# Kernel tuning notes

Hardware: AMD Instinct MI355X
Metric: run time of the kernel (lower is better)

The kernel has to match this reference:

```python
import jax, jax.numpy as jnp
import numpy as np

D_MODEL = 1024
N_HEADS = 16
D_FF = 4096
LN_EPS = 1e-5


def _layer_norm(x, g, b):
    m = jnp.mean(x, axis=-1, keepdims=True)
    v = jnp.mean((x - m) ** 2, axis=-1, keepdims=True)
    return (x - m) / jnp.sqrt(v + LN_EPS) * g + b


def setup_inputs() -> dict:
    key = jax.random.key(0)
    ks = jax.random.split(key, 16)
    s = 0.02
    d, dff = D_MODEL, D_FF
    return {
        "x": jax.random.normal(ks[0], (8, 1000, d), dtype=jnp.float32),
        # weights stored as (d_in, d_out); applied via x @ W
        "wq": jax.random.normal(ks[1], (d, d), dtype=jnp.float32) * s,
        "wk": jax.random.normal(ks[2], (d, d), dtype=jnp.float32) * s,
        "wv": jax.random.normal(ks[3], (d, d), dtype=jnp.float32) * s,
        "wo": jax.random.normal(ks[4], (d, d), dtype=jnp.float32) * s,
        "bo": jnp.zeros((d,), dtype=jnp.float32),
        "w1": jax.random.normal(ks[5], (d, dff), dtype=jnp.float32) * s,
        "b1": jnp.zeros((dff,), dtype=jnp.float32),
        "w2": jax.random.normal(ks[6], (dff, d), dtype=jnp.float32) * s,
        "b2": jnp.zeros((d,), dtype=jnp.float32),
        "g1": jnp.ones((d,), dtype=jnp.float32),
        "beta1": jnp.zeros((d,), dtype=jnp.float32),
        "g2": jnp.ones((d,), dtype=jnp.float32),
        "beta2": jnp.zeros((d,), dtype=jnp.float32),
    }


def reference(x, wq, wk, wv, wo, bo, w1, b1, w2, b2, g1, beta1, g2, beta2):
    B, S, D = x.shape
    H = N_HEADS
    dk = D // H

    # --- pre-norm attention ---
    h = _layer_norm(x, g1, beta1)
    q = (h @ wq).reshape(B, S, H, dk)
    k = (h @ wk).reshape(B, S, H, dk)
    v = (h @ wv).reshape(B, S, H, dk)
    scores = jnp.einsum('bqhd,bkhd->bhqk', q, k) / jnp.sqrt(jnp.float32(dk))
    mask = jnp.tril(jnp.ones((S, S), dtype=bool))  # causal
    scores = jnp.where(mask, scores, -jnp.inf)
    attn = jax.nn.softmax(scores, axis=-1)
    attended = jnp.einsum('bhqk,bkhd->bqhd', attn, v).reshape(B, S, D)
    x = x + attended @ wo + bo

    # --- pre-norm FFN (exact GELU, matching torch F.gelu default) ---
    h2 = _layer_norm(x, g2, beta2)
    ff = jax.nn.gelu(h2 @ w1 + b1, approximate=False) @ w2 + b2
    return x + ff
```

## Files before the change

### kernel.cpp

```cpp
#include <hip/hip_runtime.h>
#include <hip/hip_bf16.h>
#include <math.h>

#define D_MODEL 1024
#define D_FF    4096
#define N_HEADS 16
#define SEQ     1000
#define BATCH   8
#define M_TOK   (BATCH * SEQ)

typedef __bf16 bf16x8_t __attribute__((ext_vector_type(8)));
typedef short  short8_t __attribute__((ext_vector_type(8)));
typedef float  f32x4_t  __attribute__((ext_vector_type(4)));

__device__ __forceinline__ f32x4_t mfma_bf16(short8_t a, short8_t b, f32x4_t c) {
    return __builtin_amdgcn_mfma_f32_16x16x32_bf16(
        __builtin_bit_cast(bf16x8_t, a), __builtin_bit_cast(bf16x8_t, b), c, 0, 0, 0);
}

__device__ __forceinline__ unsigned short f2bf(float f) {
    union { float f; unsigned u; } x; x.f = f;
    unsigned r = (x.u + 0x7fffu + ((x.u >> 16) & 1u)) >> 16;
    return (unsigned short)r;
}

__device__ __forceinline__ float gelu_fast(float v) {
    float z = 1.5957691216f * v * fmaf(0.044715f, v * v, 1.0f);
    float e = __expf(-z);
    return v * __builtin_amdgcn_rcpf(1.0f + e);
}

__device__ __forceinline__ void gload_lds16(const void* g, void* l) {
    __builtin_amdgcn_global_load_lds(
        (const __attribute__((address_space(1))) unsigned int*)g,
        (__attribute__((address_space(3))) unsigned int*)l, 16, 0, 0);
}

__global__ __launch_bounds__(256) void prep_kernel(
    const float* __restrict__ wq, const float* __restrict__ wk,
    const float* __restrict__ wv, const float* __restrict__ wo,
    const float* __restrict__ w1, const float* __restrict__ w2,
    unsigned short* __restrict__ wqt, unsigned short* __restrict__ wkt,
    unsigned short* __restrict__ wvt, unsigned short* __restrict__ wot,
    unsigned short* __restrict__ w1t, unsigned short* __restrict__ w2t,
    const float* __restrict__ x, const float* __restrict__ g1,
    const float* __restrict__ beta1, unsigned short* __restrict__ h1) {
    int id = blockIdx.x;
    __shared__ float tile[32][33];
    __shared__ float red[8];
    if (id >= 12288) {
        int row = id - 12288, tid = threadIdx.x;
        const float4 v = ((const float4*)(x + (size_t)row * D_MODEL))[tid];
        float s  = v.x + v.y + v.z + v.w;
        float s2 = v.x * v.x + v.y * v.y + v.z * v.z + v.w * v.w;
#pragma unroll
        for (int o = 32; o > 0; o >>= 1) { s += __shfl_xor(s, o, 64); s2 += __shfl_xor(s2, o, 64); }
        int wave = tid >> 6, lane = tid & 63;
        if (lane == 0) { red[wave] = s; red[wave + 4] = s2; }
        __syncthreads();
        s  = red[0] + red[1] + red[2] + red[3];
        s2 = red[4] + red[5] + red[6] + red[7];
        float mean = s * (1.0f / D_MODEL);
        float var  = s2 * (1.0f / D_MODEL) - mean * mean;
        float rstd = rsqrtf(var + 1e-5f);
        float4 gg = ((const float4*)g1)[tid];
        float4 bb = ((const float4*)beta1)[tid];
        ushort4 o4;
        o4.x = f2bf((v.x - mean) * rstd * gg.x + bb.x);
        o4.y = f2bf((v.y - mean) * rstd * gg.y + bb.y);
        o4.z = f2bf((v.z - mean) * rstd * gg.z + bb.z);
        o4.w = f2bf((v.w - mean) * rstd * gg.w + bb.w);
        ((ushort4*)(h1 + (size_t)row * D_MODEL))[tid] = o4;
        return;
    }
    const float* w; unsigned short* wt; int Kd, Nd, bx, by;
    if (id < 4096) {
        int z = id >> 10, t = id & 1023;
        w  = z == 0 ? wq  : z == 1 ? wk  : z == 2 ? wv  : wo;
        wt = z == 0 ? wqt : z == 1 ? wkt : z == 2 ? wvt : wot;
        Kd = 1024; Nd = 1024; bx = t & 31; by = t >> 5;
    } else if (id < 8192) {
        int t = id - 4096;
        w = w1; wt = w1t; Kd = 1024; Nd = 4096; bx = t & 127; by = t >> 7;
    } else {
        int t = id - 8192;
        w = w2; wt = w2t; Kd = 4096; Nd = 1024; bx = t & 31; by = t >> 5;
    }
    int n0 = bx * 32, k0 = by * 32;
    int tx = threadIdx.x & 31, ty = threadIdx.x >> 5;
#pragma unroll
    for (int i = 0; i < 4; ++i)
        tile[ty + i * 8][tx] = w[(size_t)(k0 + ty + i * 8) * Nd + n0 + tx];
    __syncthreads();
#pragma unroll
    for (int i = 0; i < 4; ++i)
        wt[(size_t)(n0 + ty + i * 8) * Kd + k0 + tx] = f2bf(tile[tx][ty + i * 8]);
}

__global__ __launch_bounds__(256) void vtrans_kernel(const unsigned short* __restrict__ v,
                                                     unsigned short* __restrict__ vt) {
    __shared__ unsigned short tile[32][33];
    int b = blockIdx.z;
    int c0 = blockIdx.x * 32, s0 = blockIdx.y * 32;
    int tx = threadIdx.x, ty = threadIdx.y;
#pragma unroll
    for (int i = 0; i < 4; ++i) {
        int s = s0 + ty + i * 8;
        unsigned short val = 0;
        if (s < SEQ) val = v[((size_t)b * SEQ + s) * D_MODEL + c0 + tx];
        tile[ty + i * 8][tx] = val;
    }
    __syncthreads();
#pragma unroll
    for (int i = 0; i < 4; ++i) {
        int c = c0 + ty + i * 8;
        vt[((size_t)b * D_MODEL + c) * 1024 + s0 + tx] = tile[tx][ty + i * 8];
    }
}

__global__ __launch_bounds__(256) void ln_kernel(const float* __restrict__ x,
                                                 const float* __restrict__ g,
                                                 const float* __restrict__ beta,
                                                 unsigned short* __restrict__ out) {
    int row = blockIdx.x, tid = threadIdx.x;
    const float4 v = ((const float4*)(x + (size_t)row * D_MODEL))[tid];
    float s  = v.x + v.y + v.z + v.w;
    float s2 = v.x * v.x + v.y * v.y + v.z * v.z + v.w * v.w;
#pragma unroll
    for (int o = 32; o > 0; o >>= 1) { s += __shfl_xor(s, o, 64); s2 += __shfl_xor(s2, o, 64); }
    __shared__ float red[8];
    int wave = tid >> 6, lane = tid & 63;
    if (lane == 0) { red[wave] = s; red[wave + 4] = s2; }
    __syncthreads();
    s  = red[0] + red[1] + red[2] + red[3];
    s2 = red[4] + red[5] + red[6] + red[7];
    float mean = s * (1.0f / D_MODEL);
    float var  = s2 * (1.0f / D_MODEL) - mean * mean;
    float rstd = rsqrtf(var + 1e-5f);
    float4 gg = ((const float4*)g)[tid];
    float4 bb = ((const float4*)beta)[tid];
    ushort4 o4;
    o4.x = f2bf((v.x - mean) * rstd * gg.x + bb.x);
    o4.y = f2bf((v.y - mean) * rstd * gg.y + bb.y);
    o4.z = f2bf((v.z - mean) * rstd * gg.z + bb.z);
    o4.w = f2bf((v.w - mean) * rstd * gg.w + bb.w);
    ((ushort4*)(out + (size_t)row * D_MODEL))[tid] = o4;
}

enum { EPI_BF16 = 0, EPI_GELU = 1, EPI_RES_F32 = 2 };

template <int EPI, int KDIM, bool FUSE3>
__global__ __launch_bounds__(256) void gemm_bt(
    const unsigned short* __restrict__ A,
    const unsigned short* __restrict__ Bt0,
    const unsigned short* __restrict__ Bt1,
    const unsigned short* __restrict__ Bt2,
    const float* __restrict__ bias,
    const float* __restrict__ resid,
    void* __restrict__ out0, void* out1, void* out2,
    int Mdim, int Ndim) {
    constexpr int K = KDIM;
    constexpr int NKT = K / 64;
    __shared__ unsigned short lda[2][128 * 64];
    __shared__ unsigned short ldb[2][128 * 64];
    int tid = threadIdx.x;
    int lane = tid & 63, wave = tid >> 6;
    int l15 = lane & 15, quad = lane >> 4;
    int rt = blockIdx.y * 128;
    const unsigned short* Bt = Bt0;
    void* outp = out0;
    int ct;
    if (FUSE3) {
        int sel = blockIdx.x >> 3;
        ct = (blockIdx.x & 7) * 128;
        Bt   = sel == 0 ? Bt0  : (sel == 1 ? Bt1  : Bt2);
        outp = sel == 0 ? out0 : (sel == 1 ? out1 : out2);
    } else {
        ct = blockIdx.x * 128;
    }
    int wr = (wave >> 1) * 64, wc = (wave & 1) * 64;
    f32x4_t acc[4][4] = {};

    const unsigned short* ag[4];
    const unsigned short* bg[4];
#pragma unroll
    for (int i = 0; i < 4; ++i) {
        int gidx = tid + i * 256;
        int row = gidx >> 3, cp = gidx & 7;
        int c = cp ^ (row & 7);
        int ar = rt + row; if (ar >= Mdim) ar = Mdim - 1;
        ag[i] = A  + (size_t)ar * K + c * 8;
        bg[i] = Bt + (size_t)(ct + row) * K + c * 8;
    }

    auto stage = [&](int kt, int bufi) {
#pragma unroll
        for (int i = 0; i < 4; ++i) {
            gload_lds16(ag[i] + kt * 64, (char*)lda[bufi] + (wave * 64 + i * 256) * 16);
            gload_lds16(bg[i] + kt * 64, (char*)ldb[bufi] + (wave * 64 + i * 256) * 16);
        }
    };

    stage(0, 0);
    for (int kt = 0; kt < NKT; ++kt) {
        int bufi = kt & 1;
        __syncthreads();
        if (kt + 1 < NKT) stage(kt + 1, bufi ^ 1);
        const unsigned short* la = lda[bufi];
        const unsigned short* lb = ldb[bufi];
#pragma unroll
        for (int kc = 0; kc < 2; ++kc) {
            short8_t af[4], bfr[4];
#pragma unroll
            for (int mi = 0; mi < 4; ++mi) {
                int ra = wr + mi * 16 + l15;
                int cg = (kc * 4 + quad) ^ (ra & 7);
                af[mi] = *(const short8_t*)(la + (ra * 8 + cg) * 8);
            }
#pragma unroll
            for (int ni = 0; ni < 4; ++ni) {
                int rb = wc + ni * 16 + l15;
                int cg = (kc * 4 + quad) ^ (rb & 7);
                bfr[ni] = *(const short8_t*)(lb + (rb * 8 + cg) * 8);
            }
#pragma unroll
            for (int mi = 0; mi < 4; ++mi)
#pragma unroll
                for (int ni = 0; ni < 4; ++ni)
                    acc[mi][ni] = mfma_bf16(af[mi], bfr[ni], acc[mi][ni]);
        }
    }

    float bias_c[4];
    if (EPI != EPI_BF16) {
#pragma unroll
        for (int ni = 0; ni < 4; ++ni) bias_c[ni] = bias[ct + wc + ni * 16 + l15];
    }

#pragma unroll
    for (int mi = 0; mi < 4; ++mi) {
#pragma unroll
        for (int r = 0; r < 4; ++r) {
            int grow = rt + wr + mi * 16 + quad * 4 + r;
            if (grow >= Mdim) continue;
#pragma unroll
            for (int ni = 0; ni < 4; ++ni) {
                int gcol = ct + wc + ni * 16 + l15;
                float v = acc[mi][ni][r];
                size_t idx = (size_t)grow * Ndim + gcol;
                if (EPI == EPI_BF16) {
                    ((unsigned short*)outp)[idx] = f2bf(v);
                } else if (EPI == EPI_GELU) {
                    v += bias_c[ni];
                    ((unsigned short*)outp)[idx] = f2bf(gelu_fast(v));
                } else {
                    v += bias_c[ni] + resid[idx];
                    ((float*)outp)[idx] = v;
                }
            }
        }
    }
}

__global__ __launch_bounds__(256) void attn_kernel(
    const unsigned short* __restrict__ q,
    const unsigned short* __restrict__ k,
    const unsigned short* __restrict__ vt,
    unsigned short* __restrict__ att) {
    int p = blockIdx.x, h = blockIdx.y, b = blockIdx.z;
    int tid = threadIdx.x, lane = tid & 63, wave = tid >> 6;
    int l15 = lane & 15, quad = lane >> 4;
    __shared__ unsigned short kt_lds[2][64 * 64];
    __shared__ unsigned short vt_lds[2][64 * 64];
    __shared__ unsigned short p_lds[4][32 * 64];
    unsigned short* pw = p_lds[wave];

    const int qtA = p, qtB = 7 - p;
    const int tA = 2 * qtA + 2, tB = 2 * qtB + 2, total = tA + tB;

    short8_t aq[2][2][2];
#pragma unroll
    for (int ph = 0; ph < 2; ++ph) {
        int qw = (ph ? qtB : qtA) * 128 + wave * 32;
#pragma unroll
        for (int g = 0; g < 2; ++g) {
            int qr = qw + g * 16 + l15; if (qr > SEQ - 1) qr = SEQ - 1;
            const unsigned short* qp = q + ((size_t)(b * SEQ + qr)) * D_MODEL + h * 64 + quad * 8;
            aq[ph][g][0] = *(const short8_t*)qp;
            aq[ph][g][1] = *(const short8_t*)(qp + 32);
        }
    }

    f32x4_t o[2][4] = {};
    float m_run[2] = {-3.0e38f, -3.0e38f};
    float l_run[2] = {0.f, 0.f};

    auto stage = [&](int kt, int bufi) {
#pragma unroll
        for (int i = 0; i < 2; ++i) {
            int g2 = tid + i * 256;
            int row = g2 >> 3, cp = g2 & 7;
            int c = cp ^ (row & 7);
            int key = kt * 64 + row; int keyc = key < SEQ ? key : SEQ - 1;
            gload_lds16(k + ((size_t)(b * SEQ + keyc)) * D_MODEL + h * 64 + c * 8,
                        (char*)kt_lds[bufi] + (size_t)(wave * 64 + i * 256) * 16);
            gload_lds16(vt + ((size_t)((b * N_HEADS + h) * 64 + row)) * 1024 + kt * 64 + c * 8,
                        (char*)vt_lds[bufi] + (size_t)(wave * 64 + i * 256) * 16);
        }
    };

    auto flush = [&](int qt) {
#pragma unroll
        for (int g = 0; g < 2; ++g) {
            float linv = __builtin_amdgcn_rcpf(l_run[g]);
#pragma unroll
            for (int r = 0; r < 4; ++r) {
                float nr = __shfl(linv, quad * 4 + r, 64);
                int qg = qt * 128 + wave * 32 + g * 16 + quad * 4 + r;
                if (qg >= SEQ) continue;
#pragma unroll
                for (int db = 0; db < 4; ++db)
                    att[((size_t)(b * SEQ + qg)) * D_MODEL + h * 64 + db * 16 + l15] =
                        f2bf(o[g][db][r] * nr);
            }
        }
#pragma unroll
        for (int g = 0; g < 2; ++g) {
            m_run[g] = -3.0e38f; l_run[g] = 0.f;
#pragma unroll
            for (int db = 0; db < 4; ++db) o[g][db] = f32x4_t{0.f, 0.f, 0.f, 0.f};
        }
    };

    stage(0, 0);

    for (int i = 0; i < total; ++i) {
        int bufi = i & 1;
        __syncthreads();
        if (i + 1 < total) {
            int nkt = (i + 1 < tA) ? (i + 1) : (i + 1 - tA);
            stage(nkt, bufi ^ 1);
        }
        int phase = (i < tA) ? 0 : 1;
        int kt = (i < tA) ? i : i - tA;
        int qt = phase ? qtB : qtA;
        int qw = qt * 128 + wave * 32;
        const unsigned short* kl = kt_lds[bufi];
        const unsigned short* vl = vt_lds[bufi];

        if (kt * 64 <= qw + 31) {
            short8_t kf[4][2];
#pragma unroll
            for (int nb = 0; nb < 4; ++nb)
#pragma unroll
                for (int kc = 0; kc < 2; ++kc) {
                    int row = nb * 16 + l15;
                    kf[nb][kc] = *(const short8_t*)(kl + (row * 8 + ((kc * 4 + quad) ^ (row & 7))) * 8);
                }

            bool gact[2];
#pragma unroll
            for (int g = 0; g < 2; ++g) {
                gact[g] = (kt * 64 <= qw + g * 16 + 15);
                if (!gact[g]) continue;
                f32x4_t s[4] = {};
#pragma unroll
                for (int nb = 0; nb < 4; ++nb)
#pragma unroll
                    for (int kc = 0; kc < 2; ++kc)
                        s[nb] = mfma_bf16(kf[nb][kc], aq[phase][g][kc], s[nb]);
                int qrow = qw + g * 16 + l15;
                float sc[4][4];
#pragma unroll
                for (int nb = 0; nb < 4; ++nb)
#pragma unroll
                    for (int r = 0; r < 4; ++r) {
                        int key = kt * 64 + nb * 16 + quad * 4 + r;
                        float v = s[nb][r] * 0.125f;
                        sc[nb][r] = (key <= qrow) ? v : -1e30f;
                    }
                float mx = sc[0][0];
#pragma unroll
                for (int nb = 0; nb < 4; ++nb)
#pragma unroll
                    for (int r = 0; r < 4; ++r) mx = fmaxf(mx, sc[nb][r]);
                mx = fmaxf(mx, __shfl_xor(mx, 16, 64));
                mx = fmaxf(mx, __shfl_xor(mx, 32, 64));
                float mnew = fmaxf(m_run[g], mx);
                float alpha = __expf(m_run[g] - mnew);
                m_run[g] = mnew;
                float rs = 0.f;
#pragma unroll
                for (int nb = 0; nb < 4; ++nb)
#pragma unroll
                    for (int r = 0; r < 4; ++r) {
                        float pv = __expf(sc[nb][r] - mnew);
                        sc[nb][r] = pv;
                        rs += pv;
                    }
                rs += __shfl_xor(rs, 16, 64);
                rs += __shfl_xor(rs, 32, 64);
                l_run[g] = l_run[g] * alpha + rs;
#pragma unroll
                for (int r = 0; r < 4; ++r) {
                    float a = __shfl(alpha, quad * 4 + r, 64);
#pragma unroll
                    for (int db = 0; db < 4; ++db) o[g][db][r] *= a;
                }
#pragma unroll
                for (int nb = 0; nb < 4; ++nb) {
                    unsigned long long pv =
                        (unsigned long long)f2bf(sc[nb][0]) |
                        ((unsigned long long)f2bf(sc[nb][1]) << 16) |
                        ((unsigned long long)f2bf(sc[nb][2]) << 32) |
                        ((unsigned long long)f2bf(sc[nb][3]) << 48);
                    int chunk = (4 * nb + quad) ^ ((l15 & 7) << 1);
                    *(unsigned long long*)(pw + (g * 16 + l15) * 64 + chunk * 4) = pv;
                }
            }
            asm volatile("s_waitcnt lgkmcnt(0)" ::: "memory");

            short8_t vf[4][2];
#pragma unroll
            for (int db = 0; db < 4; ++db)
#pragma unroll
                for (int kc = 0; kc < 2; ++kc) {
                    int row = db * 16 + l15;
                    vf[db][kc] = *(const short8_t*)(vl + (row * 8 + ((kc * 4 + quad) ^ (row & 7))) * 8);
                }
#pragma unroll
            for (int g = 0; g < 2; ++g) {
                if (!gact[g]) continue;
                short8_t ap[2];
#pragma unroll
                for (int kc = 0; kc < 2; ++kc)
                    ap[kc] = *(const short8_t*)(pw + (g * 16 + l15) * 64 +
                                                ((kc * 4 + quad) ^ (l15 & 7)) * 8);
#pragma unroll
                for (int db = 0; db < 4; ++db)
#pragma unroll
                    for (int kc = 0; kc < 2; ++kc)
                        o[g][db] = mfma_bf16(ap[kc], vf[db][kc], o[g][db]);
            }
        }

        if (i == tA - 1) flush(qtA);
    }
    flush(qtB);
}

extern "C" void kernel_launch(void* const* d_in, const int* in_sizes, int n_in,
                              void* d_out, int out_size, void* d_ws, size_t ws_size,
                              hipStream_t stream) {
    const float* x     = (const float*)d_in[0];
    const float* wq    = (const float*)d_in[1];
    const float* wk    = (const float*)d_in[2];
    const float* wv    = (const float*)d_in[3];
    const float* wo    = (const float*)d_in[4];
    const float* bo    = (const float*)d_in[5];
    const float* w1    = (const float*)d_in[6];
    const float* b1    = (const float*)d_in[7];
    const float* w2    = (const float*)d_in[8];
    const float* b2    = (const float*)d_in[9];
    const float* g1    = (const float*)d_in[10];
    const float* beta1 = (const float*)d_in[11];
    const float* g2    = (const float*)d_in[12];
    const float* beta2 = (const float*)d_in[13];
    float* out = (float*)d_out;
    char* ws = (char*)d_ws;

    const size_t SZ_MD_BF16 = (size_t)M_TOK * D_MODEL * 2;
    unsigned short* h1  = (unsigned short*)(ws);
    unsigned short* qb  = (unsigned short*)(ws + SZ_MD_BF16);
    unsigned short* kb  = (unsigned short*)(ws + 2 * SZ_MD_BF16);
    unsigned short* vb  = (unsigned short*)(ws + 3 * SZ_MD_BF16);
    unsigned short* atb = (unsigned short*)(ws + 4 * SZ_MD_BF16);
    unsigned short* ffb = qb;
    size_t off = 5 * SZ_MD_BF16;
    unsigned short* vtb = (unsigned short*)(ws + off); off += (size_t)BATCH * D_MODEL * 1024 * 2;
    float* x1 = (float*)(ws + off); off += (size_t)M_TOK * D_MODEL * 4;
    unsigned short* wqt = (unsigned short*)(ws + off); off += (size_t)D_MODEL * D_MODEL * 2;
    unsigned short* wkt = (unsigned short*)(ws + off); off += (size_t)D_MODEL * D_MODEL * 2;
    unsigned short* wvt = (unsigned short*)(ws + off); off += (size_t)D_MODEL * D_MODEL * 2;
    unsigned short* wot = (unsigned short*)(ws + off); off += (size_t)D_MODEL * D_MODEL * 2;
    unsigned short* w1t = (unsigned short*)(ws + off); off += (size_t)D_MODEL * D_FF * 2;
    unsigned short* w2t = (unsigned short*)(ws + off); off += (size_t)D_MODEL * D_FF * 2;

    prep_kernel<<<12288 + M_TOK, 256, 0, stream>>>(
        wq, wk, wv, wo, w1, w2, wqt, wkt, wvt, wot, w1t, w2t, x, g1, beta1, h1);

    const int MT = (M_TOK + 127) / 128;
    gemm_bt<EPI_BF16, D_MODEL, true><<<dim3(24, MT), 256, 0, stream>>>(
        h1, wqt, wkt, wvt, nullptr, nullptr, qb, kb, vb, M_TOK, D_MODEL);

    dim3 tb(32, 8);
    vtrans_kernel<<<dim3(32, 32, 8), tb, 0, stream>>>(vb, vtb);

    attn_kernel<<<dim3(4, N_HEADS, BATCH), 256, 0, stream>>>(qb, kb, vtb, atb);

    gemm_bt<EPI_RES_F32, D_MODEL, false><<<dim3(8, MT), 256, 0, stream>>>(
        atb, wot, nullptr, nullptr, bo, x, x1, nullptr, nullptr, M_TOK, D_MODEL);

    ln_kernel<<<M_TOK, 256, 0, stream>>>(x1, g2, beta2, h1);

    gemm_bt<EPI_GELU, D_MODEL, false><<<dim3(32, MT), 256, 0, stream>>>(
        h1, w1t, nullptr, nullptr, b1, nullptr, ffb, nullptr, nullptr, M_TOK, D_FF);

    gemm_bt<EPI_RES_F32, D_FF, false><<<dim3(8, MT), 256, 0, stream>>>(
        ffb, w2t, nullptr, nullptr, b2, x1, out, nullptr, nullptr, M_TOK, D_MODEL);
}
```

Baseline: 512.0 us.

## Add 256x256-tile 512-thread GEMM with 4-stage LDS pipeline for QKV and FFN

Introduces a new GEMM kernel with 256x256 output tiles, 8 waves, a 4-deep direct-to-LDS prefetch ring and XOR-swizzled LDS layout. It uses s_setprio around the MFMA bursts. It replaces the 128-row-tile GEMM for the fused QKV projection and both FFN matmuls, to raise arithmetic intensity per loaded tile. The risks are fewer blocks on the grid, only 128 for the FFN2 GEMM on a 256-CU part, and more padding waste on the last M tile.

```diff
diff --git a/kernel.cpp b/kernel.cpp
--- a/kernel.cpp
+++ b/kernel.cpp
@@ -262,6 +262,137 @@
     }
 }
 
+template <int EPI, bool FUSE3>
+__global__ __launch_bounds__(512, 2) void gemm256(
+    const unsigned short* __restrict__ A,
+    const unsigned short* __restrict__ Bt0,
+    const unsigned short* __restrict__ Bt1,
+    const unsigned short* __restrict__ Bt2,
+    const float* __restrict__ bias,
+    const float* __restrict__ resid,
+    void* __restrict__ out0, void* out1, void* out2,
+    int Mdim, int Ndim, int K) {
+    __shared__ unsigned short lds[4][2][256 * 32];
+    int tid = threadIdx.x;
+    int lane = tid & 63, wave = tid >> 6;
+    int l15 = lane & 15, quad = lane >> 4;
+    int wr = wave >> 2;
+    int wc = wave & 3;
+    int rt = blockIdx.y * 256;
+    const unsigned short* Bt = Bt0;
+    void* outp = out0;
+    int ct;
+    if (FUSE3) {
+        int sel = blockIdx.x >> 2;
+        ct = (blockIdx.x & 3) * 256;
+        Bt   = sel == 0 ? Bt0  : (sel == 1 ? Bt1  : Bt2);
+        outp = sel == 0 ? out0 : (sel == 1 ? out1 : out2);
+    } else {
+        ct = blockIdx.x * 256;
+    }
+
+    const unsigned short* aS[2];
+    const unsigned short* bS[2];
+#pragma unroll
+    for (int j = 0; j < 2; ++j) {
+        int gl = tid + j * 512;
+        int p = gl >> 3, slot = gl & 7;
+        int sp = slot ^ (p & 7);
+        int rrow = 2 * p + (sp >> 2), g2 = sp & 3;
+        int ar = rt + rrow; if (ar >= Mdim) ar = Mdim - 1;
+        aS[j] = A  + (size_t)ar * K + g2 * 8;
+        bS[j] = Bt + (size_t)(ct + rrow) * K + g2 * 8;
+    }
+    auto stageA = [&](int kt) {
+        char* base = (char*)&lds[kt & 3][0][0];
+#pragma unroll
+        for (int j = 0; j < 2; ++j)
+            gload_lds16(aS[j] + (size_t)kt * 32, base + (wave * 64 + j * 512) * 16);
+    };
+    auto stageB = [&](int kt) {
+        char* base = (char*)&lds[kt & 3][1][0];
+#pragma unroll
+        for (int j = 0; j < 2; ++j)
+            gload_lds16(bS[j] + (size_t)kt * 32, base + (wave * 64 + j * 512) * 16);
+    };
+
+    int lh = l15 >> 1;
+    int mslot = (quad + ((l15 & 1) << 2)) ^ lh;
+    unsigned aOff = (unsigned)((wr * 64 + lh) * 128 + mslot * 16);
+    unsigned bOff = (unsigned)((wc * 32 + lh) * 128 + mslot * 16);
+
+    f32x4_t acc[8][4] = {};
+    int NT = K >> 5;
+
+    stageA(0); stageB(0); stageA(1); stageB(1); stageA(2); stageB(2);
+
+    for (int t = 0; t < NT; ++t) {
+        int sl = t & 3;
+        asm volatile("s_waitcnt vmcnt(8)" ::: "memory");
+        __builtin_amdgcn_s_barrier();
+        const char* la = (const char*)&lds[sl][0][0];
+        const char* lb = (const char*)&lds[sl][1][0];
+        short8_t af[4], bfv[4];
+#pragma unroll
+        for (int mi = 0; mi < 4; ++mi)
+            af[mi] = *(const short8_t*)(la + aOff + mi * 1024);
+#pragma unroll
+        for (int ni = 0; ni < 4; ++ni)
+            bfv[ni] = *(const short8_t*)(lb + bOff + ni * 1024);
+        if (t + 3 < NT) stageA(t + 3);
+        __builtin_amdgcn_s_setprio(1);
+#pragma unroll
+        for (int mi = 0; mi < 4; ++mi)
+#pragma unroll
+            for (int ni = 0; ni < 4; ++ni)
+                acc[mi][ni] = mfma_bf16(af[mi], bfv[ni], acc[mi][ni]);
+        __builtin_amdgcn_s_setprio(0);
+        asm volatile("" ::: "memory");
+        __builtin_amdgcn_s_barrier();
+#pragma unroll
+        for (int mi = 0; mi < 4; ++mi)
+            af[mi] = *(const short8_t*)(la + aOff + 4096 + mi * 1024);
+        if (t + 3 < NT) stageB(t + 3);
+        __builtin_amdgcn_s_setprio(1);
+#pragma unroll
+        for (int mi = 0; mi < 4; ++mi)
+#pragma unroll
+            for (int ni = 0; ni < 4; ++ni)
+                acc[4 + mi][ni] = mfma_bf16(af[mi], bfv[ni], acc[4 + mi][ni]);
+        __builtin_amdgcn_s_setprio(0);
+    }
+
+    float bias_c[4];
+    if (EPI != EPI_BF16) {
+#pragma unroll
+        for (int ni = 0; ni < 4; ++ni) bias_c[ni] = bias[ct + wc * 64 + ni * 16 + l15];
+    }
+
+#pragma unroll
+    for (int mi = 0; mi < 8; ++mi) {
+#pragma unroll
+        for (int r = 0; r < 4; ++r) {
+            int grow = rt + wr * 128 + mi * 16 + quad * 4 + r;
+            if (grow >= Mdim) continue;
+#pragma unroll
+            for (int ni = 0; ni < 4; ++ni) {
+                int gcol = ct + wc * 64 + ni * 16 + l15;
+                float v = acc[mi][ni][r];
+                size_t idx = (size_t)grow * Ndim + gcol;
+                if (EPI == EPI_BF16) {
+                    ((unsigned short*)outp)[idx] = f2bf(v);
+                } else if (EPI == EPI_GELU) {
+                    v += bias_c[ni];
+                    ((unsigned short*)outp)[idx] = f2bf(gelu_fast(v));
+                } else {
+                    v += bias_c[ni] + resid[idx];
+                    ((float*)outp)[idx] = v;
+                }
+            }
+        }
+    }
+}
+
 __global__ __launch_bounds__(256) void attn_kernel(
     const unsigned short* __restrict__ q,
     const unsigned short* __restrict__ k,
@@ -489,23 +620,25 @@
     prep_kernel<<<12288 + M_TOK, 256, 0, stream>>>(
         wq, wk, wv, wo, w1, w2, wqt, wkt, wvt, wot, w1t, w2t, x, g1, beta1, h1);
 
-    const int MT = (M_TOK + 127) / 128;
-    gemm_bt<EPI_BF16, D_MODEL, true><<<dim3(24, MT), 256, 0, stream>>>(
-        h1, wqt, wkt, wvt, nullptr, nullptr, qb, kb, vb, M_TOK, D_MODEL);
+    const int MT128 = (M_TOK + 127) / 128;
+    const int MT256 = (M_TOK + 255) / 256;
+
+    gemm256<EPI_BF16, true><<<dim3(12, MT256), 512, 0, stream>>>(
+        h1, wqt, wkt, wvt, nullptr, nullptr, qb, kb, vb, M_TOK, D_MODEL, D_MODEL);
 
     dim3 tb(32, 8);
     vtrans_kernel<<<dim3(32, 32, 8), tb, 0, stream>>>(vb, vtb);
 
     attn_kernel<<<dim3(4, N_HEADS, BATCH), 256, 0, stream>>>(qb, kb, vtb, atb);
 
-    gemm_bt<EPI_RES_F32, D_MODEL, false><<<dim3(8, MT), 256, 0, stream>>>(
+    gemm_bt<EPI_RES_F32, D_MODEL, false><<<dim3(8, MT128), 256, 0, stream>>>(
         atb, wot, nullptr, nullptr, bo, x, x1, nullptr, nullptr, M_TOK, D_MODEL);
 
     ln_kernel<<<M_TOK, 256, 0, stream>>>(x1, g2, beta2, h1);
 
-    gemm_bt<EPI_GELU, D_MODEL, false><<<dim3(32, MT), 256, 0, stream>>>(
-        h1, w1t, nullptr, nullptr, b1, nullptr, ffb, nullptr, nullptr, M_TOK, D_FF);
-
-    gemm_bt<EPI_RES_F32, D_FF, false><<<dim3(8, MT), 256, 0, stream>>>(
-        ffb, w2t, nullptr, nullptr, b2, x1, out, nullptr, nullptr, M_TOK, D_MODEL);
-}
+    gemm256<EPI_GELU, false><<<dim3(16, MT256), 512, 0, stream>>>(
+        h1, w1t, nullptr, nullptr, b1, nullptr, ffb, nullptr, nullptr, M_TOK, D_FF, D_MODEL);
+
+    gemm256<EPI_RES_F32, false><<<dim3(4, MT256), 512, 0, stream>>>(
+        ffb, w2t, nullptr, nullptr, b2, x1, out, nullptr, nullptr, M_TOK, D_MODEL, D_FF);
+}
```

After: 504.3 us. About the same (-1.5%).

## Replace GEMM with 128x256-tile, 512-thread kernel using 6-stage LDS pipeline

Applied to the files above, without the earlier changes.

Replaces the 128x128 double-buffered GEMM with a 128x256 tile computed by 8 waves, using a six-slot ring of K=32 LDS stages filled by direct global-to-LDS loads. Explicit vmcnt waits and raw barriers keep loads four stages ahead, and s_setprio raises priority around the MFMA burst. The aim is to hide global load latency and increase per-block reuse of A. The larger tile reduces grid size and raises LDS use, which could limit occupancy or leave tail imbalance.

```diff
diff --git a/kernel.cpp b/kernel.cpp
--- a/kernel.cpp
+++ b/kernel.cpp
@@ -149,8 +149,8 @@
 
 enum { EPI_BF16 = 0, EPI_GELU = 1, EPI_RES_F32 = 2 };
 
-template <int EPI, int KDIM, bool FUSE3>
-__global__ __launch_bounds__(256) void gemm_bt(
+template <int EPI, bool FUSE3>
+__global__ __launch_bounds__(512, 2) void gemm128p(
     const unsigned short* __restrict__ A,
     const unsigned short* __restrict__ Bt0,
     const unsigned short* __restrict__ Bt1,
@@ -158,94 +158,115 @@
     const float* __restrict__ bias,
     const float* __restrict__ resid,
     void* __restrict__ out0, void* out1, void* out2,
-    int Mdim, int Ndim) {
-    constexpr int K = KDIM;
-    constexpr int NKT = K / 64;
-    __shared__ unsigned short lda[2][128 * 64];
-    __shared__ unsigned short ldb[2][128 * 64];
+    int Mdim, int Ndim, int K) {
+    __shared__ unsigned short ldsA[6][128 * 32];
+    __shared__ unsigned short ldsB[6][256 * 32];
     int tid = threadIdx.x;
     int lane = tid & 63, wave = tid >> 6;
     int l15 = lane & 15, quad = lane >> 4;
+    int wr = wave >> 2;
+    int wc = wave & 3;
     int rt = blockIdx.y * 128;
     const unsigned short* Bt = Bt0;
     void* outp = out0;
     int ct;
     if (FUSE3) {
-        int sel = blockIdx.x >> 3;
-        ct = (blockIdx.x & 7) * 128;
+        int sel = blockIdx.x >> 2;
+        ct = (blockIdx.x & 3) * 256;
         Bt   = sel == 0 ? Bt0  : (sel == 1 ? Bt1  : Bt2);
         outp = sel == 0 ? out0 : (sel == 1 ? out1 : out2);
     } else {
-        ct = blockIdx.x * 128;
-    }
-    int wr = (wave >> 1) * 64, wc = (wave & 1) * 64;
+        ct = blockIdx.x * 256;
+    }
+
+    const unsigned short* aSrc;
+    {
+        int p = tid >> 3, sp = (tid & 7) ^ (p & 7);
+        int rrow = 2 * p + (sp >> 2), g2 = sp & 3;
+        int ar = rt + rrow; if (ar >= Mdim) ar = Mdim - 1;
+        aSrc = A + (size_t)ar * K + g2 * 8;
+    }
+    const unsigned short* bSrc[2];
+#pragma unroll
+    for (int j = 0; j < 2; ++j) {
+        int gl = tid + j * 512;
+        int p = gl >> 3, sp = (gl & 7) ^ (p & 7);
+        int rrow = 2 * p + (sp >> 2), g2 = sp & 3;
+        bSrc[j] = Bt + (size_t)(ct + rrow) * K + g2 * 8;
+    }
+    auto stage = [&](int kt, int sl) {
+        gload_lds16(aSrc + (size_t)kt * 32, (char*)ldsA[sl] + wave * 1024);
+        gload_lds16(bSrc[0] + (size_t)kt * 32, (char*)ldsB[sl] + wave * 1024);
+        gload_lds16(bSrc[1] + (size_t)kt * 32, (char*)ldsB[sl] + 8192 + wave * 1024);
+    };
+
+    int lh = l15 >> 1;
+    int mslot = (quad + ((l15 & 1) << 2)) ^ lh;
+    unsigned aOff = (unsigned)((wr * 32 + lh) * 128 + mslot * 16);
+    unsigned bOff = (unsigned)((wc * 32 + lh) * 128 + mslot * 16);
+
     f32x4_t acc[4][4] = {};
-
-    const unsigned short* ag[4];
-    const unsigned short* bg[4];
-#pragma unroll
-    for (int i = 0; i < 4; ++i) {
-        int gidx = tid + i * 256;
-        int row = gidx >> 3, cp = gidx & 7;
-        int c = cp ^ (row & 7);
-        int ar = rt + row; if (ar >= Mdim) ar = Mdim - 1;
-        ag[i] = A  + (size_t)ar * K + c * 8;
-        bg[i] = Bt + (size_t)(ct + row) * K + c * 8;
-    }
-
-    auto stage = [&](int kt, int bufi) {
-#pragma unroll
-        for (int i = 0; i < 4; ++i) {
-            gload_lds16(ag[i] + kt * 64, (char*)lda[bufi] + (wave * 64 + i * 256) * 16);
-            gload_lds16(bg[i] + kt * 64, (char*)ldb[bufi] + (wave * 64 + i * 256) * 16);
-        }
-    };
-
-    stage(0, 0);
-    for (int kt = 0; kt < NKT; ++kt) {
-        int bufi = kt & 1;
-        __syncthreads();
-        if (kt + 1 < NKT) stage(kt + 1, bufi ^ 1);
-        const unsigned short* la = lda[bufi];
-        const unsigned short* lb = ldb[bufi];
-#pragma unroll
-        for (int kc = 0; kc < 2; ++kc) {
-            short8_t af[4], bfr[4];
-#pragma unroll
-            for (int mi = 0; mi < 4; ++mi) {
-                int ra = wr + mi * 16 + l15;
-                int cg = (kc * 4 + quad) ^ (ra & 7);
-                af[mi] = *(const short8_t*)(la + (ra * 8 + cg) * 8);
-            }
-#pragma unroll
-            for (int ni = 0; ni < 4; ++ni) {
-                int rb = wc + ni * 16 + l15;
-                int cg = (kc * 4 + quad) ^ (rb & 7);
-                bfr[ni] = *(const short8_t*)(lb + (rb * 8 + cg) * 8);
-            }
-#pragma unroll
-            for (int mi = 0; mi < 4; ++mi)
-#pragma unroll
-                for (int ni = 0; ni < 4; ++ni)
-                    acc[mi][ni] = mfma_bf16(af[mi], bfr[ni], acc[mi][ni]);
-        }
+    int NT = K >> 5;
+
+    stage(0, 0); stage(1, 1); stage(2, 2); stage(3, 3);
+
+    int s0 = 0;
+    for (int t = 0; t < NT; t += 2) {
+        int s1 = s0 + 1;
+        int s4 = (s0 >= 2) ? s0 - 2 : s0 + 4;
+        int s5 = s4 + 1;
+        if (t + 2 < NT) asm volatile("s_waitcnt vmcnt(6)" ::: "memory");
+        else            asm volatile("s_waitcnt vmcnt(0)" ::: "memory");
+        __builtin_amdgcn_s_barrier();
+        const char* la0 = (const char*)ldsA[s0];
+        const char* lb0 = (const char*)ldsB[s0];
+        const char* la1 = (const char*)ldsA[s1];
+        const char* lb1 = (const char*)ldsB[s1];
+        short8_t af0[4], bf0[4], af1[4], bf1[4];
+#pragma unroll
+        for (int mi = 0; mi < 4; ++mi)
+            af0[mi] = *(const short8_t*)(la0 + aOff + mi * 1024);
+#pragma unroll
+        for (int ni = 0; ni < 4; ++ni)
+            bf0[ni] = *(const short8_t*)(lb0 + bOff + ni * 1024);
+        if (t + 4 < NT) stage(t + 4, s4);
+#pragma unroll
+        for (int mi = 0; mi < 4; ++mi)
+            af1[mi] = *(const short8_t*)(la1 + aOff + mi * 1024);
+#pragma unroll
+        for (int ni = 0; ni < 4; ++ni)
+            bf1[ni] = *(const short8_t*)(lb1 + bOff + ni * 1024);
+        if (t + 5 < NT) stage(t + 5, s5);
+        __builtin_amdgcn_s_setprio(1);
+#pragma unroll
+        for (int mi = 0; mi < 4; ++mi)
+#pragma unroll
+            for (int ni = 0; ni < 4; ++ni)
+                acc[mi][ni] = mfma_bf16(af0[mi], bf0[ni], acc[mi][ni]);
+#pragma unroll
+        for (int mi = 0; mi < 4; ++mi)
+#pragma unroll
+            for (int ni = 0; ni < 4; ++ni)
+                acc[mi][ni] = mfma_bf16(af1[mi], bf1[ni], acc[mi][ni]);
+        __builtin_amdgcn_s_setprio(0);
+        s0 += 2; if (s0 >= 6) s0 -= 6;
     }
 
     float bias_c[4];
     if (EPI != EPI_BF16) {
 #pragma unroll
-        for (int ni = 0; ni < 4; ++ni) bias_c[ni] = bias[ct + wc + ni * 16 + l15];
+        for (int ni = 0; ni < 4; ++ni) bias_c[ni] = bias[ct + wc * 64 + ni * 16 + l15];
     }
 
 #pragma unroll
     for (int mi = 0; mi < 4; ++mi) {
 #pragma unroll
         for (int r = 0; r < 4; ++r) {
-            int grow = rt + wr + mi * 16 + quad * 4 + r;
+            int grow = rt + wr * 64 + mi * 16 + quad * 4 + r;
             if (grow >= Mdim) continue;
 #pragma unroll
             for (int ni = 0; ni < 4; ++ni) {
-                int gcol = ct + wc + ni * 16 + l15;
+                int gcol = ct + wc * 64 + ni * 16 + l15;
                 float v = acc[mi][ni][r];
                 size_t idx = (size_t)grow * Ndim + gcol;
                 if (EPI == EPI_BF16) {
@@ -489,23 +510,24 @@
     prep_kernel<<<12288 + M_TOK, 256, 0, stream>>>(
         wq, wk, wv, wo, w1, w2, wqt, wkt, wvt, wot, w1t, w2t, x, g1, beta1, h1);
 
-    const int MT = (M_TOK + 127) / 128;
-    gemm_bt<EPI_BF16, D_MODEL, true><<<dim3(24, MT), 256, 0, stream>>>(
-        h1, wqt, wkt, wvt, nullptr, nullptr, qb, kb, vb, M_TOK, D_MODEL);
+    const int MT128 = (M_TOK + 127) / 128;
+
+    gemm128p<EPI_BF16, true><<<dim3(12, MT128), 512, 0, stream>>>(
+        h1, wqt, wkt, wvt, nullptr, nullptr, qb, kb, vb, M_TOK, D_MODEL, D_MODEL);
 
     dim3 tb(32, 8);
     vtrans_kernel<<<dim3(32, 32, 8), tb, 0, stream>>>(vb, vtb);
 
     attn_kernel<<<dim3(4, N_HEADS, BATCH), 256, 0, stream>>>(qb, kb, vtb, atb);
 
-    gemm_bt<EPI_RES_F32, D_MODEL, false><<<dim3(8, MT), 256, 0, stream>>>(
-        atb, wot, nullptr, nullptr, bo, x, x1, nullptr, nullptr, M_TOK, D_MODEL);
+    gemm128p<EPI_RES_F32, false><<<dim3(4, MT128), 512, 0, stream>>>(
+        atb, wot, nullptr, nullptr, bo, x, x1, nullptr, nullptr, M_TOK, D_MODEL, D_MODEL);
 
     ln_kernel<<<M_TOK, 256, 0, stream>>>(x1, g2, beta2, h1);
 
-    gemm_bt<EPI_GELU, D_MODEL, false><<<dim3(32, MT), 256, 0, stream>>>(
-        h1, w1t, nullptr, nullptr, b1, nullptr, ffb, nullptr, nullptr, M_TOK, D_FF);
-
-    gemm_bt<EPI_RES_F32, D_FF, false><<<dim3(8, MT), 256, 0, stream>>>(
-        ffb, w2t, nullptr, nullptr, b2, x1, out, nullptr, nullptr, M_TOK, D_MODEL);
-}
+    gemm128p<EPI_GELU, false><<<dim3(16, MT128), 512, 0, stream>>>(
+        h1, w1t, nullptr, nullptr, b1, nullptr, ffb, nullptr, nullptr, M_TOK, D_FF, D_MODEL);
+
+    gemm128p<EPI_RES_F32, false><<<dim3(4, MT128), 512, 0, stream>>>(
+        ffb, w2t, nullptr, nullptr, b2, x1, out, nullptr, nullptr, M_TOK, D_MODEL, D_FF);
+}
```

New measurement: 514.3 us. About the same (+0.4%).
